# Performance work log

Hardware: AMD Instinct MI355X
Metric: run time of the kernel (lower is better)

The kernel has to match this reference:

```python
import jax, jax.numpy as jnp
import numpy as np
from jax import lax

INPUT_SCALE = 1.0
RES_SCALE = 1.0


def setup_inputs() -> dict:
    key = jax.random.key(0)
    k1, k2, k3, k4 = jax.random.split(key, 4)
    seq_len, input_size, res_size = 4096, 512, 2048
    return {
        "input_data": jax.random.normal(k1, (seq_len, input_size), dtype=jnp.float32),
        "initial_state": jax.random.normal(k2, (res_size,), dtype=jnp.float32),
        "W_in": jax.random.normal(k3, (res_size, input_size), dtype=jnp.float32),
        "W_res": jax.random.normal(k4, (res_size, res_size), dtype=jnp.float32),
    }


def reference(input_data, initial_state, W_in, W_res):
    # state_t = tanh(input_scale * W_in @ x_t + res_scale * W_res @ state_{t-1}) / sqrt(res_size)
    res_size = W_res.shape[0]
    inv_sqrt = jnp.asarray(1.0 / np.sqrt(res_size), dtype=input_data.dtype)
    # Precompute input projection for all timesteps as one GEMM: (seq_len, res_size)
    pre = (INPUT_SCALE * input_data) @ W_in.T

    def step(state, u_t):
        new_state = jnp.tanh(u_t + RES_SCALE * (W_res @ state)) * inv_sqrt
        return new_state, new_state

    _, states = lax.scan(step, initial_state, pre)
    # (seq_len + 1, res_size): row 0 is the initial state
    return jnp.concatenate([initial_state[None, :], states], axis=0)
```

## Files before the change

kernel.cpp:

```cpp
#include <hip/hip_runtime.h>

constexpr int SEQ  = 4096;
constexpr int IN   = 512;
constexpr int RS   = 2048;
constexpr int GB   = 64;
constexpr int BT   = 512;
constexpr int RING = 8;
constexpr float INV_SQRT = 0.022097086912079612f;

__global__ __launch_bounds__(256)
void gemm_pre_kernel(const float* __restrict__ A, const float* __restrict__ B,
                     float* __restrict__ out) {
    __shared__ float As[64][17];
    __shared__ float Bs[64][17];
    const int tid = threadIdx.x;
    const int tx = tid & 15, ty = tid >> 4;
    const int m0 = blockIdx.x * 64, n0 = blockIdx.y * 64;
    const int lr = tid >> 2;
    const int lk = (tid & 3) * 4;
    float acc[4][4] = {};
    for (int k0 = 0; k0 < IN; k0 += 16) {
        const float4 av = *(const float4*)&A[(size_t)(m0 + lr) * IN + k0 + lk];
        const float4 bv = *(const float4*)&B[(size_t)(n0 + lr) * IN + k0 + lk];
        __syncthreads();
        As[lr][lk + 0] = av.x; As[lr][lk + 1] = av.y;
        As[lr][lk + 2] = av.z; As[lr][lk + 3] = av.w;
        Bs[lr][lk + 0] = bv.x; Bs[lr][lk + 1] = bv.y;
        Bs[lr][lk + 2] = bv.z; Bs[lr][lk + 3] = bv.w;
        __syncthreads();
#pragma unroll
        for (int k = 0; k < 16; ++k) {
            float a[4], b[4];
#pragma unroll
            for (int i = 0; i < 4; ++i) a[i] = As[ty * 4 + i][k];
#pragma unroll
            for (int j = 0; j < 4; ++j) b[j] = Bs[tx * 4 + j][k];
#pragma unroll
            for (int i = 0; i < 4; ++i)
#pragma unroll
                for (int j = 0; j < 4; ++j) acc[i][j] += a[i] * b[j];
        }
    }
#pragma unroll
    for (int i = 0; i < 4; ++i) {
        float4 v = make_float4(acc[i][0], acc[i][1], acc[i][2], acc[i][3]);
        *(float4*)&out[(size_t)(m0 + ty * 4 + i + 1) * RS + n0 + tx * 4] = v;
    }
}

__device__ __forceinline__ float fast_tanh(float x) {
    float e = __expf(2.0f * x);
    return 1.0f - 2.0f * __builtin_amdgcn_rcpf(e + 1.0f);
}

typedef unsigned long long u64;
#define AT_LOAD_U64(p)     __hip_atomic_load((p), __ATOMIC_RELAXED, __HIP_MEMORY_SCOPE_AGENT)
#define AT_STORE_U32(p, v) __hip_atomic_store((p), (v), __ATOMIC_RELAXED, __HIP_MEMORY_SCOPE_AGENT)

__global__ __launch_bounds__(BT, 2)
void reservoir_scan_kernel(const float* __restrict__ W_res,
                           const float* __restrict__ init,
                           float* __restrict__ out,
                           unsigned* __restrict__ ring32) {
    __shared__ float s_state[RS];
    __shared__ float s_pub[32];
    u64* ring = (u64*)ring32;
    const int bid  = blockIdx.x;
    const int tid  = threadIdx.x;
    const int wave = tid >> 6;
    const int lane = tid & 63;
    const int r0   = bid * 32 + wave * 4;

    float4 w[4][8];
#pragma unroll
    for (int r = 0; r < 4; ++r) {
        const float* wp = W_res + (size_t)(r0 + r) * RS + lane * 4;
#pragma unroll
        for (int j = 0; j < 8; ++j) w[r][j] = *(const float4*)(wp + j * 256);
    }
#pragma unroll
    for (int r = 0; r < 4; ++r)
#pragma unroll
        for (int j = 0; j < 8; ++j)
            asm volatile("" : "+v"(w[r][j].x), "+v"(w[r][j].y),
                              "+v"(w[r][j].z), "+v"(w[r][j].w));

    if (wave == 0 && lane < 32) {
        float v = init[bid * 32 + lane];
        out[bid * 32 + lane] = v;
        s_pub[lane] = v;
        AT_STORE_U32(ring32 + bid * 32 + lane, __float_as_uint(v) | 1u);
    }
    __syncthreads();

    for (int t = 0; t < SEQ; ++t) {
        const size_t crow = (size_t)(t & (RING - 1)) * (RS / 2);
        const size_t prow = (size_t)((t + 1) & (RING - 1)) * RS;
        const unsigned tag_c = ((unsigned)(t >> 3) & 1u) ^ 1u;
        const unsigned tag_p = ((unsigned)((t + 1) >> 3) & 1u) ^ 1u;

        float pre = 0.f;
        if (lane < 4) pre = out[(size_t)(t + 1) * RS + r0 + lane];

        if ((tid >> 3) == bid) {
            const int k = tid & 7;
            *(float4*)&s_state[4 * tid] = *(const float4*)&s_pub[4 * k];
        } else {
            const u64* pp = ring + crow + 2 * tid;
            u64 v0 = AT_LOAD_U64(pp);
            u64 v1 = AT_LOAD_U64(pp + 1);
#define RDY(x) (((((unsigned)(x) ^ tag_c) | ((unsigned)((x) >> 32) ^ tag_c)) & 1u) == 0u)
            while (!(RDY(v0) && RDY(v1))) {
                v0 = AT_LOAD_U64(pp);
                v1 = AT_LOAD_U64(pp + 1);
            }
#undef RDY
            float4 sv;
            sv.x = __uint_as_float((unsigned)v0);
            sv.y = __uint_as_float((unsigned)(v0 >> 32));
            sv.z = __uint_as_float((unsigned)v1);
            sv.w = __uint_as_float((unsigned)(v1 >> 32));
            *(float4*)&s_state[4 * tid] = sv;
        }
        __syncthreads();

        float a0 = 0.f, a1 = 0.f, a2 = 0.f, a3 = 0.f;
#pragma unroll
        for (int j = 0; j < 8; ++j) {
            const float4 sv = *(const float4*)&s_state[lane * 4 + j * 256];
            a0 += w[0][j].x * sv.x + w[0][j].y * sv.y + w[0][j].z * sv.z + w[0][j].w * sv.w;
            a1 += w[1][j].x * sv.x + w[1][j].y * sv.y + w[1][j].z * sv.z + w[1][j].w * sv.w;
            a2 += w[2][j].x * sv.x + w[2][j].y * sv.y + w[2][j].z * sv.z + w[2][j].w * sv.w;
            a3 += w[3][j].x * sv.x + w[3][j].y * sv.y + w[3][j].z * sv.z + w[3][j].w * sv.w;
        }

        const bool p1 = (lane & 1) != 0;
        float k01 = p1 ? a1 : a0, s01 = p1 ? a0 : a1;
        k01 += __shfl_xor(s01, 1);
        float k23 = p1 ? a3 : a2, s23 = p1 ? a2 : a3;
        k23 += __shfl_xor(s23, 1);
        const bool p2 = (lane & 2) != 0;
        float kk = p2 ? k23 : k01, ss = p2 ? k01 : k23;
        kk += __shfl_xor(ss, 2);
        kk += __shfl_xor(kk, 4);
        kk += __shfl_xor(kk, 8);
        kk += __shfl_xor(kk, 16);
        kk += __shfl_xor(kk, 32);

        if (lane < 4) {
            float s = fast_tanh(pre + kk) * INV_SQRT;
            out[(size_t)(t + 1) * RS + r0 + lane] = s;
            s_pub[wave * 4 + lane] = s;
        }
        __syncthreads();

        if (wave == 0 && lane < 32) {
            unsigned bits = __float_as_uint(s_pub[lane]);
            AT_STORE_U32(ring32 + prow + bid * 32 + lane,
                         (bits & ~1u) | tag_p);
        }
    }
}

extern "C" void kernel_launch(void* const* d_in, const int* in_sizes, int n_in,
                              void* d_out, int out_size, void* d_ws, size_t ws_size,
                              hipStream_t stream) {
    const float* x     = (const float*)d_in[0];
    const float* init  = (const float*)d_in[1];
    const float* W_in  = (const float*)d_in[2];
    const float* W_res = (const float*)d_in[3];
    float* out = (float*)d_out;
    unsigned* ring = (unsigned*)d_ws;

    hipMemsetAsync(d_ws, 0, (size_t)RING * RS * sizeof(float), stream);
    gemm_pre_kernel<<<dim3(SEQ / 64, RS / 64), 256, 0, stream>>>(x, W_in, out);

    void* args[] = { (void*)&W_res, (void*)&init, (void*)&out, (void*)&ring };
    hipLaunchCooperativeKernel((void*)reservoir_scan_kernel,
                               dim3(GB), dim3(BT), args, 0, stream);
}
```

Before: 7.793 ms.

## Make each wave poll the global state ring directly, removing block barriers

The scan kernel is reshaped from 64 blocks of 512 threads into 256 blocks of 128 threads. Each wave now loads the full previous state straight from the tagged global ring into registers and checks readiness per chunk. This removes the shared-memory staging and both per-step __syncthreads. Each wave publishes its own four outputs as two tagged 64-bit stores. The intent is to shorten the per-timestep critical path of the sequential recurrence, at the cost of about eight times more L2/global ring traffic and polling per step, since every wave re-reads the whole state.

```diff
diff --git a/kernel.cpp b/kernel.cpp
--- a/kernel.cpp
+++ b/kernel.cpp
@@ -3,8 +3,8 @@
 constexpr int SEQ  = 4096;
 constexpr int IN   = 512;
 constexpr int RS   = 2048;
-constexpr int GB   = 64;
-constexpr int BT   = 512;
+constexpr int GB   = 256;
+constexpr int BT   = 128;
 constexpr int RING = 8;
 constexpr float INV_SQRT = 0.022097086912079612f;
 
@@ -55,21 +55,24 @@
 
 typedef unsigned long long u64;
 #define AT_LOAD_U64(p)     __hip_atomic_load((p), __ATOMIC_RELAXED, __HIP_MEMORY_SCOPE_AGENT)
-#define AT_STORE_U32(p, v) __hip_atomic_store((p), (v), __ATOMIC_RELAXED, __HIP_MEMORY_SCOPE_AGENT)
+#define AT_STORE_U64(p, v) __hip_atomic_store((p), (v), __ATOMIC_RELAXED, __HIP_MEMORY_SCOPE_AGENT)
+
+__device__ __forceinline__ u64 enc2(float a, float b, unsigned tag) {
+    return (u64)((__float_as_uint(a) & ~1u) | tag) |
+           ((u64)((__float_as_uint(b) & ~1u) | tag) << 32);
+}
 
 __global__ __launch_bounds__(BT, 2)
 void reservoir_scan_kernel(const float* __restrict__ W_res,
                            const float* __restrict__ init,
                            float* __restrict__ out,
                            unsigned* __restrict__ ring32) {
-    __shared__ float s_state[RS];
-    __shared__ float s_pub[32];
     u64* ring = (u64*)ring32;
-    const int bid  = blockIdx.x;
     const int tid  = threadIdx.x;
     const int wave = tid >> 6;
     const int lane = tid & 63;
-    const int r0   = bid * 32 + wave * 4;
+    const int gw   = blockIdx.x * (BT / 64) + wave;
+    const int r0   = gw * 4;
 
     float4 w[4][8];
 #pragma unroll
@@ -85,54 +88,51 @@
             asm volatile("" : "+v"(w[r][j].x), "+v"(w[r][j].y),
                               "+v"(w[r][j].z), "+v"(w[r][j].w));
 
-    if (wave == 0 && lane < 32) {
-        float v = init[bid * 32 + lane];
-        out[bid * 32 + lane] = v;
-        s_pub[lane] = v;
-        AT_STORE_U32(ring32 + bid * 32 + lane, __float_as_uint(v) | 1u);
+    if (lane == 0) {
+        float4 v = *(const float4*)(init + r0);
+        *(float4*)(out + r0) = v;
+        AT_STORE_U64(ring + (r0 >> 1),     enc2(v.x, v.y, 1u));
+        AT_STORE_U64(ring + (r0 >> 1) + 1, enc2(v.z, v.w, 1u));
     }
-    __syncthreads();
 
     for (int t = 0; t < SEQ; ++t) {
-        const size_t crow = (size_t)(t & (RING - 1)) * (RS / 2);
-        const size_t prow = (size_t)((t + 1) & (RING - 1)) * RS;
+        const u64* rp = ring + (size_t)(t & (RING - 1)) * (RS / 2);
+        u64*       pp = ring + (size_t)((t + 1) & (RING - 1)) * (RS / 2);
         const unsigned tag_c = ((unsigned)(t >> 3) & 1u) ^ 1u;
         const unsigned tag_p = ((unsigned)((t + 1) >> 3) & 1u) ^ 1u;
 
         float pre = 0.f;
         if (lane < 4) pre = out[(size_t)(t + 1) * RS + r0 + lane];
 
-        if ((tid >> 3) == bid) {
-            const int k = tid & 7;
-            *(float4*)&s_state[4 * tid] = *(const float4*)&s_pub[4 * k];
-        } else {
-            const u64* pp = ring + crow + 2 * tid;
-            u64 v0 = AT_LOAD_U64(pp);
-            u64 v1 = AT_LOAD_U64(pp + 1);
+        u64 q0[8], q1[8];
+#pragma unroll
+        for (int j = 0; j < 8; ++j) {
+            const u64* a = rp + 2 * lane + 128 * j;
+            q0[j] = AT_LOAD_U64(a);
+            q1[j] = AT_LOAD_U64(a + 1);
+        }
+
+        float a0 = 0.f, a1 = 0.f, a2 = 0.f, a3 = 0.f;
 #define RDY(x) (((((unsigned)(x) ^ tag_c) | ((unsigned)((x) >> 32) ^ tag_c)) & 1u) == 0u)
+#pragma unroll
+        for (int j = 0; j < 8; ++j) {
+            const u64* a = rp + 2 * lane + 128 * j;
+            u64 v0 = q0[j], v1 = q1[j];
             while (!(RDY(v0) && RDY(v1))) {
-                v0 = AT_LOAD_U64(pp);
-                v1 = AT_LOAD_U64(pp + 1);
+                v0 = AT_LOAD_U64(a);
+                v1 = AT_LOAD_U64(a + 1);
             }
-#undef RDY
             float4 sv;
             sv.x = __uint_as_float((unsigned)v0);
             sv.y = __uint_as_float((unsigned)(v0 >> 32));
             sv.z = __uint_as_float((unsigned)v1);
             sv.w = __uint_as_float((unsigned)(v1 >> 32));
-            *(float4*)&s_state[4 * tid] = sv;
-        }
-        __syncthreads();
-
-        float a0 = 0.f, a1 = 0.f, a2 = 0.f, a3 = 0.f;
-#pragma unroll
-        for (int j = 0; j < 8; ++j) {
-            const float4 sv = *(const float4*)&s_state[lane * 4 + j * 256];
             a0 += w[0][j].x * sv.x + w[0][j].y * sv.y + w[0][j].z * sv.z + w[0][j].w * sv.w;
             a1 += w[1][j].x * sv.x + w[1][j].y * sv.y + w[1][j].z * sv.z + w[1][j].w * sv.w;
             a2 += w[2][j].x * sv.x + w[2][j].y * sv.y + w[2][j].z * sv.z + w[2][j].w * sv.w;
             a3 += w[3][j].x * sv.x + w[3][j].y * sv.y + w[3][j].z * sv.z + w[3][j].w * sv.w;
         }
+#undef RDY
 
         const bool p1 = (lane & 1) != 0;
         float k01 = p1 ? a1 : a0, s01 = p1 ? a0 : a1;
@@ -147,18 +147,16 @@
         kk += __shfl_xor(kk, 16);
         kk += __shfl_xor(kk, 32);
 
+        float s = 0.f;
         if (lane < 4) {
-            float s = fast_tanh(pre + kk) * INV_SQRT;
+            s = fast_tanh(pre + kk) * INV_SQRT;
             out[(size_t)(t + 1) * RS + r0 + lane] = s;
-            s_pub[wave * 4 + lane] = s;
         }
-        __syncthreads();
 
-        if (wave == 0 && lane < 32) {
-            unsigned bits = __float_as_uint(s_pub[lane]);
-            AT_STORE_U32(ring32 + prow + bid * 32 + lane,
-                         (bits & ~1u) | tag_p);
-        }
+        float pa = __shfl(s, (lane & 1) * 2);
+        float pb = __shfl(s, (lane & 1) * 2 + 1);
+        if (lane < 2)
+            AT_STORE_U64(pp + (r0 >> 1) + lane, enc2(pa, pb, tag_p));
     }
 }
 
```

After: 20.63 ms. 2.65x slower.

## Fuse input projection into persistent scan kernel, drop separate GEMM

Applied to the files above, without the earlier changes.

Removes the standalone input-projection GEMM and computes W_in·x_t inside the recurrent scan loop, with each wave holding its W_in rows in registers and loading x_t each step. The x_t load is issued before the spin-wait on the state ring so its latency can hide behind synchronization. The output store is also moved after the ring publish so it is off the critical path. The cost is more registers per thread and extra per-step FMAs on the serial critical path.

```diff
diff --git a/kernel.cpp b/kernel.cpp
--- a/kernel.cpp
+++ b/kernel.cpp
@@ -7,46 +7,6 @@
 constexpr int BT   = 512;
 constexpr int RING = 8;
 constexpr float INV_SQRT = 0.022097086912079612f;
-
-__global__ __launch_bounds__(256)
-void gemm_pre_kernel(const float* __restrict__ A, const float* __restrict__ B,
-                     float* __restrict__ out) {
-    __shared__ float As[64][17];
-    __shared__ float Bs[64][17];
-    const int tid = threadIdx.x;
-    const int tx = tid & 15, ty = tid >> 4;
-    const int m0 = blockIdx.x * 64, n0 = blockIdx.y * 64;
-    const int lr = tid >> 2;
-    const int lk = (tid & 3) * 4;
-    float acc[4][4] = {};
-    for (int k0 = 0; k0 < IN; k0 += 16) {
-        const float4 av = *(const float4*)&A[(size_t)(m0 + lr) * IN + k0 + lk];
-        const float4 bv = *(const float4*)&B[(size_t)(n0 + lr) * IN + k0 + lk];
-        __syncthreads();
-        As[lr][lk + 0] = av.x; As[lr][lk + 1] = av.y;
-        As[lr][lk + 2] = av.z; As[lr][lk + 3] = av.w;
-        Bs[lr][lk + 0] = bv.x; Bs[lr][lk + 1] = bv.y;
-        Bs[lr][lk + 2] = bv.z; Bs[lr][lk + 3] = bv.w;
-        __syncthreads();
-#pragma unroll
-        for (int k = 0; k < 16; ++k) {
-            float a[4], b[4];
-#pragma unroll
-            for (int i = 0; i < 4; ++i) a[i] = As[ty * 4 + i][k];
-#pragma unroll
-            for (int j = 0; j < 4; ++j) b[j] = Bs[tx * 4 + j][k];
-#pragma unroll
-            for (int i = 0; i < 4; ++i)
-#pragma unroll
-                for (int j = 0; j < 4; ++j) acc[i][j] += a[i] * b[j];
-        }
-    }
-#pragma unroll
-    for (int i = 0; i < 4; ++i) {
-        float4 v = make_float4(acc[i][0], acc[i][1], acc[i][2], acc[i][3]);
-        *(float4*)&out[(size_t)(m0 + ty * 4 + i + 1) * RS + n0 + tx * 4] = v;
-    }
-}
 
 __device__ __forceinline__ float fast_tanh(float x) {
     float e = __expf(2.0f * x);
@@ -58,8 +18,10 @@
 #define AT_STORE_U32(p, v) __hip_atomic_store((p), (v), __ATOMIC_RELAXED, __HIP_MEMORY_SCOPE_AGENT)
 
 __global__ __launch_bounds__(BT, 2)
-void reservoir_scan_kernel(const float* __restrict__ W_res,
+void reservoir_scan_kernel(const float* __restrict__ x,
                            const float* __restrict__ init,
+                           const float* __restrict__ W_in,
+                           const float* __restrict__ W_res,
                            float* __restrict__ out,
                            unsigned* __restrict__ ring32) {
     __shared__ float s_state[RS];
@@ -85,6 +47,20 @@
             asm volatile("" : "+v"(w[r][j].x), "+v"(w[r][j].y),
                               "+v"(w[r][j].z), "+v"(w[r][j].w));
 
+    float4 wi[4][2];
+#pragma unroll
+    for (int r = 0; r < 4; ++r) {
+        const float* wp = W_in + (size_t)(r0 + r) * IN + lane * 8;
+        wi[r][0] = *(const float4*)wp;
+        wi[r][1] = *(const float4*)(wp + 4);
+    }
+#pragma unroll
+    for (int r = 0; r < 4; ++r)
+#pragma unroll
+        for (int j = 0; j < 2; ++j)
+            asm volatile("" : "+v"(wi[r][j].x), "+v"(wi[r][j].y),
+                              "+v"(wi[r][j].z), "+v"(wi[r][j].w));
+
     if (wave == 0 && lane < 32) {
         float v = init[bid * 32 + lane];
         out[bid * 32 + lane] = v;
@@ -99,8 +75,9 @@
         const unsigned tag_c = ((unsigned)(t >> 3) & 1u) ^ 1u;
         const unsigned tag_p = ((unsigned)((t + 1) >> 3) & 1u) ^ 1u;
 
-        float pre = 0.f;
-        if (lane < 4) pre = out[(size_t)(t + 1) * RS + r0 + lane];
+        const float* xp = x + (size_t)t * IN + lane * 8;
+        float4 xv0 = *(const float4*)xp;
+        float4 xv1 = *(const float4*)(xp + 4);
 
         if ((tid >> 3) == bid) {
             const int k = tid & 7;
@@ -109,7 +86,7 @@
             const u64* pp = ring + crow + 2 * tid;
             u64 v0 = AT_LOAD_U64(pp);
             u64 v1 = AT_LOAD_U64(pp + 1);
-#define RDY(x) (((((unsigned)(x) ^ tag_c) | ((unsigned)((x) >> 32) ^ tag_c)) & 1u) == 0u)
+#define RDY(v) (((((unsigned)(v) ^ tag_c) | ((unsigned)((v) >> 32) ^ tag_c)) & 1u) == 0u)
             while (!(RDY(v0) && RDY(v1))) {
                 v0 = AT_LOAD_U64(pp);
                 v1 = AT_LOAD_U64(pp + 1);
@@ -124,7 +101,14 @@
         }
         __syncthreads();
 
-        float a0 = 0.f, a1 = 0.f, a2 = 0.f, a3 = 0.f;
+        float a0 = wi[0][0].x*xv0.x + wi[0][0].y*xv0.y + wi[0][0].z*xv0.z + wi[0][0].w*xv0.w
+                 + wi[0][1].x*xv1.x + wi[0][1].y*xv1.y + wi[0][1].z*xv1.z + wi[0][1].w*xv1.w;
+        float a1 = wi[1][0].x*xv0.x + wi[1][0].y*xv0.y + wi[1][0].z*xv0.z + wi[1][0].w*xv0.w
+                 + wi[1][1].x*xv1.x + wi[1][1].y*xv1.y + wi[1][1].z*xv1.z + wi[1][1].w*xv1.w;
+        float a2 = wi[2][0].x*xv0.x + wi[2][0].y*xv0.y + wi[2][0].z*xv0.z + wi[2][0].w*xv0.w
+                 + wi[2][1].x*xv1.x + wi[2][1].y*xv1.y + wi[2][1].z*xv1.z + wi[2][1].w*xv1.w;
+        float a3 = wi[3][0].x*xv0.x + wi[3][0].y*xv0.y + wi[3][0].z*xv0.z + wi[3][0].w*xv0.w
+                 + wi[3][1].x*xv1.x + wi[3][1].y*xv1.y + wi[3][1].z*xv1.z + wi[3][1].w*xv1.w;
 #pragma unroll
         for (int j = 0; j < 8; ++j) {
             const float4 sv = *(const float4*)&s_state[lane * 4 + j * 256];
@@ -147,10 +131,10 @@
         kk += __shfl_xor(kk, 16);
         kk += __shfl_xor(kk, 32);
 
+        float sres = 0.f;
         if (lane < 4) {
-            float s = fast_tanh(pre + kk) * INV_SQRT;
-            out[(size_t)(t + 1) * RS + r0 + lane] = s;
-            s_pub[wave * 4 + lane] = s;
+            sres = fast_tanh(kk) * INV_SQRT;
+            s_pub[wave * 4 + lane] = sres;
         }
         __syncthreads();
 
@@ -159,6 +143,9 @@
             AT_STORE_U32(ring32 + prow + bid * 32 + lane,
                          (bits & ~1u) | tag_p);
         }
+
+        if (lane < 4)
+            out[(size_t)(t + 1) * RS + r0 + lane] = sres;
     }
 }
 
@@ -173,9 +160,9 @@
     unsigned* ring = (unsigned*)d_ws;
 
     hipMemsetAsync(d_ws, 0, (size_t)RING * RS * sizeof(float), stream);
-    gemm_pre_kernel<<<dim3(SEQ / 64, RS / 64), 256, 0, stream>>>(x, W_in, out);
 
-    void* args[] = { (void*)&W_res, (void*)&init, (void*)&out, (void*)&ring };
+    void* args[] = { (void*)&x, (void*)&init, (void*)&W_in, (void*)&W_res,
+                     (void*)&out, (void*)&ring };
     hipLaunchCooperativeKernel((void*)reservoir_scan_kernel,
                                dim3(GB), dim3(BT), args, 0, stream);
 }
```

New measurement: 7.558 ms, median of 2. 1.03x faster.
